# Optimization experiments

Hardware: AMD Instinct MI355X
Metric: run time of the kernel (lower is better)

## Reference

```python
import jax, jax.numpy as jnp
import numpy as np

B, D, Nh, L = 8, 128, 8, 1024
Dk = D // Nh  # 16
Dv = D // Nh  # 16

def _xavier(key, shape):
    # nn.init.xavier_normal_ on a 3D tensor treats dim0 as fan irrelevant:
    # fan_in = shape[-1]*1, fan_out = shape[-2]*1 for >=2D; receptive field = prod(shape[2:])? For 3D torch uses
    # fan_in = shape[1]*shape[2]? We just need same distribution family; use std from last two dims.
    fan_in, fan_out = shape[-1], shape[-2]
    std = float(np.sqrt(2.0 / (fan_in + fan_out)))
    return jax.random.normal(key, shape, dtype=jnp.float32) * std

def setup_inputs() -> dict:
    key = jax.random.key(0)
    kx, kq, kk, kv, ko = jax.random.split(key, 5)
    x = jax.random.normal(kx, (B, D, L), dtype=jnp.float32)
    Wq = _xavier(kq, (Nh, B, Dk, D))
    Wk = _xavier(kk, (Nh, B, Dk, D))
    Wv = _xavier(kv, (Nh, B, Dv, D))
    Wo = _xavier(ko, (B, Dv * Nh, D))
    return {"x": x, "Wq": Wq, "Wk": Wk, "Wv": Wv, "Wo": Wo}

def reference(x, Wq, Wk, Wv, Wo):
    scale = 1.0 / np.sqrt(Dk)
    # Project all heads at once: [Nh,B,Dk,D] x [B,D,L] -> [B,Nh,Dk,L]
    Q = jnp.einsum('hbkd,bdl->bhkl', Wq, x)
    K = jnp.einsum('hbkd,bdl->bhkl', Wk, x)
    V = jnp.einsum('hbvd,bdl->bhvl', Wv, x)
    # scores[b,h,i,j] = sum_k Q[b,h,k,i] * K[b,h,k,j]
    scores = jnp.einsum('bhki,bhkj->bhij', Q, K) * scale
    # original softmaxes over dim=1 of [B,L,L] -> the i (Q-length) axis
    attn = jax.nn.softmax(scores, axis=2)
    # head[b,h,v,j] = sum_i V[b,h,v,i] * attn[b,h,i,j]
    head = jnp.einsum('bhvi,bhij->bhvj', V, attn)
    # concat heads along channel dim (order matches torch.cat over head list)
    head = head.reshape(B, Nh * Dv, L)
    # Wo [B, Nh*Dv, D] bmm head [B, D(=Nh*Dv), L] -> [B, Nh*Dv, L]
    out = jnp.einsum('bod,bdl->bol', Wo, head)
    return out
```

## Files before the change

kernel.cpp:

```cpp
#include <hip/hip_runtime.h>
#include <hip/hip_bf16.h>

#define B_ 8
#define D_ 128
#define NH 8
#define L_ 1024
#define DK 16

typedef __attribute__((ext_vector_type(4))) short s4;
typedef __attribute__((ext_vector_type(4))) float f4;

static __device__ __forceinline__ unsigned short f2bf(float f) {
    __hip_bfloat16 h = __float2bfloat16(f);
    return *reinterpret_cast<unsigned short*>(&h);
}
static __device__ __forceinline__ unsigned pack2(float a, float b) {
    return (unsigned)f2bf(a) | ((unsigned)f2bf(b) << 16);
}
static __device__ __forceinline__ s4 pack4(float a, float b, float c, float d) {
    union { unsigned u[2]; s4 v; } un;
    un.u[0] = pack2(a, b);
    un.u[1] = pack2(c, d);
    return un.v;
}

#if __has_builtin(__builtin_amdgcn_mfma_f32_16x16x16_bf16)
#define MFMA16(a, b, c) __builtin_amdgcn_mfma_f32_16x16x16_bf16(a, b, c, 0, 0, 0)
#elif __has_builtin(__builtin_amdgcn_mfma_f32_16x16x16bf16_1k)
#define MFMA16(a, b, c) __builtin_amdgcn_mfma_f32_16x16x16bf16_1k(a, b, c, 0, 0, 0)
#else
static __device__ __forceinline__ f4 mfma16_asm(s4 a, s4 b, f4 c) {
    f4 d;
    asm volatile("v_mfma_f32_16x16x16_bf16 %0, %1, %2, %3"
                 : "=&v"(d) : "v"(a), "v"(b), "v"(c));
    return d;
}
#define MFMA16(a, b, c) mfma16_asm(a, b, c)
#endif

__global__ __launch_bounds__(256)
void proj_kernel(const float* __restrict__ x,
                 const float* __restrict__ Wq,
                 const float* __restrict__ Wk,
                 const float* __restrict__ Wv,
                 unsigned short* __restrict__ Qt,
                 unsigned short* __restrict__ Kt,
                 unsigned short* __restrict__ Vt) {
    const int lane = threadIdx.x & 63;
    const int wv   = threadIdx.x >> 6;
    const int m = lane & 15, q = lane >> 4;
    const int bh = blockIdx.y, b = bh >> 3, h = bh & 7;
    const int which = blockIdx.z;
    const int n0 = (blockIdx.x * 4 + wv) * 32;

    const float* W = (which == 0) ? Wq : (which == 1) ? Wk : Wv;
    const float* Wrow = W + ((size_t)((h * B_ + b) * DK + m)) * D_;
    const float* xb = x + (size_t)b * D_ * L_ + n0 + m;

    f4 acc0 = {0.f, 0.f, 0.f, 0.f}, acc1 = {0.f, 0.f, 0.f, 0.f};
#pragma unroll
    for (int kb = 0; kb < 8; ++kb) {
        const int k4 = kb * 16 + q * 4;
        float4 wf = *(const float4*)(Wrow + k4);
        s4 a = pack4(wf.x, wf.y, wf.z, wf.w);

        const float* xc = xb + (size_t)k4 * L_;
        float b00 = xc[0];          float b01 = xc[L_];
        float b02 = xc[2 * L_];     float b03 = xc[3 * L_];
        float b10 = xc[16];         float b11 = xc[L_ + 16];
        float b12 = xc[2 * L_ + 16];float b13 = xc[3 * L_ + 16];
        s4 bf0 = pack4(b00, b01, b02, b03);
        s4 bf1 = pack4(b10, b11, b12, b13);

        acc0 = MFMA16(a, bf0, acc0);
        acc1 = MFMA16(a, bf1, acc1);
    }

    if (which == 2) {
        unsigned short* vp = Vt + ((size_t)bh * DK + q * 4) * L_ + n0 + m;
        vp[0]      = f2bf(acc0[0]); vp[L_]     = f2bf(acc0[1]);
        vp[2 * L_] = f2bf(acc0[2]); vp[3 * L_] = f2bf(acc0[3]);
        vp += 16;
        vp[0]      = f2bf(acc1[0]); vp[L_]     = f2bf(acc1[1]);
        vp[2 * L_] = f2bf(acc1[2]); vp[3 * L_] = f2bf(acc1[3]);
    } else {
        const float sc = (which == 1) ? 0.25f : 1.0f;
        unsigned short* T = (which == 0) ? Qt : Kt;
        uint2 u0, u1;
        u0.x = pack2(acc0[0] * sc, acc0[1] * sc);
        u0.y = pack2(acc0[2] * sc, acc0[3] * sc);
        u1.x = pack2(acc1[0] * sc, acc1[1] * sc);
        u1.y = pack2(acc1[2] * sc, acc1[3] * sc);
        *(uint2*)(T + ((size_t)bh * L_ + n0 + m) * DK + q * 4)      = u0;
        *(uint2*)(T + ((size_t)bh * L_ + n0 + 16 + m) * DK + q * 4) = u1;
    }
}

__global__ __launch_bounds__(256)
void attn_out_kernel(const unsigned short* __restrict__ Qt,
                     const unsigned short* __restrict__ Kt,
                     const unsigned short* __restrict__ Vt,
                     const float* __restrict__ Wo,
                     float* __restrict__ out) {
    const int lane = threadIdx.x & 63;
    const int wv   = threadIdx.x >> 6;
    const int m = lane & 15, q = lane >> 4;
    const int b    = blockIdx.y;
    const int jblk = blockIdx.x * 32;

    __shared__ unsigned short hls[32][132];

#pragma unroll
    for (int hh = 0; hh < 2; ++hh) {
        const int h  = wv + hh * 4;
        const int bh = b * NH + h;

        s4 bk0 = *(const s4*)(Kt + ((size_t)bh * L_ + jblk + m) * DK + q * 4);
        s4 bk1 = *(const s4*)(Kt + ((size_t)bh * L_ + jblk + 16 + m) * DK + q * 4);

        f4 O0 = {0.f, 0.f, 0.f, 0.f}, O1 = {0.f, 0.f, 0.f, 0.f};
        float ls0 = 0.f, ls1 = 0.f;
        const unsigned short* qbase = Qt + (size_t)bh * L_ * DK + q * 4;
        const unsigned short* vbase = Vt + ((size_t)bh * DK + m) * L_ + q * 4;

#pragma unroll 4
        for (int i0 = 0; i0 < L_; i0 += 16) {
            s4 aq = *(const s4*)(qbase + (size_t)(i0 + m) * DK);
            s4 av = *(const s4*)(vbase + i0);

            f4 z = {0.f, 0.f, 0.f, 0.f};
            f4 S0 = MFMA16(aq, bk0, z);
            f4 S1 = MFMA16(aq, bk1, z);

            float p00 = __expf(S0[0]), p01 = __expf(S0[1]);
            float p02 = __expf(S0[2]), p03 = __expf(S0[3]);
            float p10 = __expf(S1[0]), p11 = __expf(S1[1]);
            float p12 = __expf(S1[2]), p13 = __expf(S1[3]);
            ls0 += (p00 + p01) + (p02 + p03);
            ls1 += (p10 + p11) + (p12 + p13);

            s4 pb0, pb1;
            pb0[0] = (short)f2bf(p00); pb0[1] = (short)f2bf(p01);
            pb0[2] = (short)f2bf(p02); pb0[3] = (short)f2bf(p03);
            pb1[0] = (short)f2bf(p10); pb1[1] = (short)f2bf(p11);
            pb1[2] = (short)f2bf(p12); pb1[3] = (short)f2bf(p13);

            O0 = MFMA16(av, pb0, O0);
            O1 = MFMA16(av, pb1, O1);
        }

        ls0 += __shfl_xor(ls0, 16, 64);
        ls0 += __shfl_xor(ls0, 32, 64);
        ls1 += __shfl_xor(ls1, 16, 64);
        ls1 += __shfl_xor(ls1, 32, 64);
        const float inv0 = 1.f / ls0, inv1 = 1.f / ls1;

        uint2 o0, o1;
        o0.x = pack2(O0[0] * inv0, O0[1] * inv0);
        o0.y = pack2(O0[2] * inv0, O0[3] * inv0);
        o1.x = pack2(O1[0] * inv1, O1[1] * inv1);
        o1.y = pack2(O1[2] * inv1, O1[3] * inv1);
        *(uint2*)&hls[m][h * 16 + q * 4]      = o0;
        *(uint2*)&hls[16 + m][h * 16 + q * 4] = o1;
    }

    __syncthreads();

#pragma unroll
    for (int t = 0; t < 2; ++t) {
        const int oc = wv * 2 + t;
        const int o0 = oc * 16;
        const float* Wrow = Wo + ((size_t)b * D_ + o0 + m) * D_;

        f4 acc0 = {0.f, 0.f, 0.f, 0.f}, acc1 = {0.f, 0.f, 0.f, 0.f};
#pragma unroll
        for (int kb = 0; kb < 8; ++kb) {
            const int k4 = kb * 16 + q * 4;
            float4 wf = *(const float4*)(Wrow + k4);
            s4 a  = pack4(wf.x, wf.y, wf.z, wf.w);
            s4 b0 = *(const s4*)&hls[m][k4];
            s4 b1 = *(const s4*)&hls[16 + m][k4];
            acc0 = MFMA16(a, b0, acc0);
            acc1 = MFMA16(a, b1, acc1);
        }

        float* op = out + ((size_t)b * D_ + o0 + q * 4) * L_ + jblk + m;
        op[0]      = acc0[0]; op[L_]     = acc0[1];
        op[2 * L_] = acc0[2]; op[3 * L_] = acc0[3];
        op += 16;
        op[0]      = acc1[0]; op[L_]     = acc1[1];
        op[2 * L_] = acc1[2]; op[3 * L_] = acc1[3];
    }
}

extern "C" void kernel_launch(void* const* d_in, const int* in_sizes, int n_in,
                              void* d_out, int out_size, void* d_ws, size_t ws_size,
                              hipStream_t stream) {
    const float* x  = (const float*)d_in[0];
    const float* Wq = (const float*)d_in[1];
    const float* Wk = (const float*)d_in[2];
    const float* Wv = (const float*)d_in[3];
    const float* Wo = (const float*)d_in[4];
    float* out = (float*)d_out;

    const size_t SEG = (size_t)B_ * NH * DK * L_;
    unsigned short* Qt = (unsigned short*)d_ws;
    unsigned short* Kt = Qt + SEG;
    unsigned short* Vt = Kt + SEG;

    proj_kernel<<<dim3(8, B_ * NH, 3), 256, 0, stream>>>(x, Wq, Wk, Wv, Qt, Kt, Vt);
    attn_out_kernel<<<dim3(32, B_), 256, 0, stream>>>(Qt, Kt, Vt, Wo, out);
}
```

Baseline: 103.7 us.

## Split attention reduction across 16 waves per block and use exp2 with prescaled K

```diff
diff --git a/kernel.cpp b/kernel.cpp
--- a/kernel.cpp
+++ b/kernel.cpp
@@ -22,6 +22,14 @@
     un.u[0] = pack2(a, b);
     un.u[1] = pack2(c, d);
     return un.v;
+}
+
+static __device__ __forceinline__ float fexp2(float x) {
+#if __has_builtin(__builtin_amdgcn_exp2f)
+    return __builtin_amdgcn_exp2f(x);
+#else
+    float r; asm("v_exp_f32 %0, %1" : "=v"(r) : "v"(x)); return r;
+#endif
 }
 
 #if __has_builtin(__builtin_amdgcn_mfma_f32_16x16x16_bf16)
@@ -84,7 +92,7 @@
         vp[0]      = f2bf(acc1[0]); vp[L_]     = f2bf(acc1[1]);
         vp[2 * L_] = f2bf(acc1[2]); vp[3 * L_] = f2bf(acc1[3]);
     } else {
-        const float sc = (which == 1) ? 0.25f : 1.0f;
+        const float sc = (which == 1) ? 0.25f * 1.4426950408889634f : 1.0f;
         unsigned short* T = (which == 0) ? Qt : Kt;
         uint2 u0, u1;
         u0.x = pack2(acc0[0] * sc, acc0[1] * sc);
@@ -96,64 +104,79 @@
     }
 }
 
-__global__ __launch_bounds__(256)
+__global__ __launch_bounds__(1024)
 void attn_out_kernel(const unsigned short* __restrict__ Qt,
                      const unsigned short* __restrict__ Kt,
                      const unsigned short* __restrict__ Vt,
                      const float* __restrict__ Wo,
                      float* __restrict__ out) {
     const int lane = threadIdx.x & 63;
-    const int wv   = threadIdx.x >> 6;
+    const int wid  = threadIdx.x >> 6;
     const int m = lane & 15, q = lane >> 4;
     const int b    = blockIdx.y;
     const int jblk = blockIdx.x * 32;
 
+    const int h     = wid & 7;
+    const int ihalf = wid >> 3;
+    const int bh    = b * NH + h;
+
     __shared__ unsigned short hls[32][132];
-
-#pragma unroll
-    for (int hh = 0; hh < 2; ++hh) {
-        const int h  = wv + hh * 4;
-        const int bh = b * NH + h;
-
-        s4 bk0 = *(const s4*)(Kt + ((size_t)bh * L_ + jblk + m) * DK + q * 4);
-        s4 bk1 = *(const s4*)(Kt + ((size_t)bh * L_ + jblk + 16 + m) * DK + q * 4);
-
-        f4 O0 = {0.f, 0.f, 0.f, 0.f}, O1 = {0.f, 0.f, 0.f, 0.f};
-        float ls0 = 0.f, ls1 = 0.f;
-        const unsigned short* qbase = Qt + (size_t)bh * L_ * DK + q * 4;
-        const unsigned short* vbase = Vt + ((size_t)bh * DK + m) * L_ + q * 4;
+    __shared__ float red[8][64][12];
+
+    s4 bk0 = *(const s4*)(Kt + ((size_t)bh * L_ + jblk + m) * DK + q * 4);
+    s4 bk1 = *(const s4*)(Kt + ((size_t)bh * L_ + jblk + 16 + m) * DK + q * 4);
+
+    f4 O0 = {0.f, 0.f, 0.f, 0.f}, O1 = {0.f, 0.f, 0.f, 0.f};
+    float ls0 = 0.f, ls1 = 0.f;
+    const unsigned short* qbase = Qt + (size_t)bh * L_ * DK + q * 4
+                                     + (size_t)(ihalf * (L_ / 2)) * DK;
+    const unsigned short* vbase = Vt + ((size_t)bh * DK + m) * L_ + q * 4
+                                     + ihalf * (L_ / 2);
 
 #pragma unroll 4
-        for (int i0 = 0; i0 < L_; i0 += 16) {
-            s4 aq = *(const s4*)(qbase + (size_t)(i0 + m) * DK);
-            s4 av = *(const s4*)(vbase + i0);
-
-            f4 z = {0.f, 0.f, 0.f, 0.f};
-            f4 S0 = MFMA16(aq, bk0, z);
-            f4 S1 = MFMA16(aq, bk1, z);
-
-            float p00 = __expf(S0[0]), p01 = __expf(S0[1]);
-            float p02 = __expf(S0[2]), p03 = __expf(S0[3]);
-            float p10 = __expf(S1[0]), p11 = __expf(S1[1]);
-            float p12 = __expf(S1[2]), p13 = __expf(S1[3]);
-            ls0 += (p00 + p01) + (p02 + p03);
-            ls1 += (p10 + p11) + (p12 + p13);
-
-            s4 pb0, pb1;
-            pb0[0] = (short)f2bf(p00); pb0[1] = (short)f2bf(p01);
-            pb0[2] = (short)f2bf(p02); pb0[3] = (short)f2bf(p03);
-            pb1[0] = (short)f2bf(p10); pb1[1] = (short)f2bf(p11);
-            pb1[2] = (short)f2bf(p12); pb1[3] = (short)f2bf(p13);
-
-            O0 = MFMA16(av, pb0, O0);
-            O1 = MFMA16(av, pb1, O1);
-        }
-
-        ls0 += __shfl_xor(ls0, 16, 64);
-        ls0 += __shfl_xor(ls0, 32, 64);
-        ls1 += __shfl_xor(ls1, 16, 64);
-        ls1 += __shfl_xor(ls1, 32, 64);
-        const float inv0 = 1.f / ls0, inv1 = 1.f / ls1;
+    for (int i0 = 0; i0 < L_ / 2; i0 += 16) {
+        s4 aq = *(const s4*)(qbase + (size_t)(i0 + m) * DK);
+        s4 av = *(const s4*)(vbase + i0);
+
+        f4 z = {0.f, 0.f, 0.f, 0.f};
+        f4 S0 = MFMA16(aq, bk0, z);
+        f4 S1 = MFMA16(aq, bk1, z);
+
+        float p00 = fexp2(S0[0]), p01 = fexp2(S0[1]);
+        float p02 = fexp2(S0[2]), p03 = fexp2(S0[3]);
+        float p10 = fexp2(S1[0]), p11 = fexp2(S1[1]);
+        float p12 = fexp2(S1[2]), p13 = fexp2(S1[3]);
+        ls0 += (p00 + p01) + (p02 + p03);
+        ls1 += (p10 + p11) + (p12 + p13);
+
+        s4 pb0, pb1;
+        pb0[0] = (short)f2bf(p00); pb0[1] = (short)f2bf(p01);
+        pb0[2] = (short)f2bf(p02); pb0[3] = (short)f2bf(p03);
+        pb1[0] = (short)f2bf(p10); pb1[1] = (short)f2bf(p11);
+        pb1[2] = (short)f2bf(p12); pb1[3] = (short)f2bf(p13);
+
+        O0 = MFMA16(av, pb0, O0);
+        O1 = MFMA16(av, pb1, O1);
+    }
+
+    ls0 += __shfl_xor(ls0, 16, 64);
+    ls0 += __shfl_xor(ls0, 32, 64);
+    ls1 += __shfl_xor(ls1, 16, 64);
+    ls1 += __shfl_xor(ls1, 32, 64);
+
+    if (ihalf) {
+        float* r = red[h][lane];
+        *(f4*)(r)     = O0;
+        *(f4*)(r + 4) = O1;
+        r[8] = ls0; r[9] = ls1;
+    }
+    __syncthreads();
+    if (!ihalf) {
+        const float* r = red[h][lane];
+        f4 P0 = *(const f4*)(r), P1 = *(const f4*)(r + 4);
+        O0 += P0; O1 += P1;
+        const float inv0 = 1.f / (ls0 + r[8]);
+        const float inv1 = 1.f / (ls1 + r[9]);
 
         uint2 o0, o1;
         o0.x = pack2(O0[0] * inv0, O0[1] * inv0);
@@ -163,33 +186,26 @@
         *(uint2*)&hls[m][h * 16 + q * 4]      = o0;
         *(uint2*)&hls[16 + m][h * 16 + q * 4] = o1;
     }
-
     __syncthreads();
 
-#pragma unroll
-    for (int t = 0; t < 2; ++t) {
-        const int oc = wv * 2 + t;
+    {
+        const int oc = wid & 7, jt = wid >> 3;
         const int o0 = oc * 16;
         const float* Wrow = Wo + ((size_t)b * D_ + o0 + m) * D_;
 
-        f4 acc0 = {0.f, 0.f, 0.f, 0.f}, acc1 = {0.f, 0.f, 0.f, 0.f};
+        f4 acc = {0.f, 0.f, 0.f, 0.f};
 #pragma unroll
         for (int kb = 0; kb < 8; ++kb) {
             const int k4 = kb * 16 + q * 4;
             float4 wf = *(const float4*)(Wrow + k4);
             s4 a  = pack4(wf.x, wf.y, wf.z, wf.w);
-            s4 b0 = *(const s4*)&hls[m][k4];
-            s4 b1 = *(const s4*)&hls[16 + m][k4];
-            acc0 = MFMA16(a, b0, acc0);
-            acc1 = MFMA16(a, b1, acc1);
+            s4 bb = *(const s4*)&hls[jt * 16 + m][k4];
+            acc = MFMA16(a, bb, acc);
         }
 
-        float* op = out + ((size_t)b * D_ + o0 + q * 4) * L_ + jblk + m;
-        op[0]      = acc0[0]; op[L_]     = acc0[1];
-        op[2 * L_] = acc0[2]; op[3 * L_] = acc0[3];
-        op += 16;
-        op[0]      = acc1[0]; op[L_]     = acc1[1];
-        op[2 * L_] = acc1[2]; op[3 * L_] = acc1[3];
+        float* op = out + ((size_t)b * D_ + o0 + q * 4) * L_ + jblk + jt * 16 + m;
+        op[0]      = acc[0]; op[L_]     = acc[1];
+        op[2 * L_] = acc[2]; op[3 * L_] = acc[3];
     }
 }
 
@@ -209,5 +225,5 @@
     unsigned short* Vt = Kt + SEG;
 
     proj_kernel<<<dim3(8, B_ * NH, 3), 256, 0, stream>>>(x, Wq, Wk, Wv, Qt, Kt, Vt);
-    attn_out_kernel<<<dim3(32, B_), 256, 0, stream>>>(Qt, Kt, Vt, Wo, out);
-}
+    attn_out_kernel<<<dim3(32, B_), 1024, 0, stream>>>(Qt, Kt, Vt, Wo, out);
+}
```

New measurement: 99.58 us. 1.04x faster.
